# Optimization experiments

Measured on AMD Instinct MI355X. Metric: run time of the kernel, lower is better.

## Reference

```python
import jax, jax.numpy as jnp
import numpy as np
import math

D_MODEL = 256
NUM_SLOTS = 128
RANK = 32
STEPS = 6
VOCAB = 32000
SEQ = 512
BATCH = 8
LN_EPS = 1e-5


def setup_inputs() -> dict:
    key = jax.random.key(0)
    ks = jax.random.split(key, 16)
    std = 0.02
    inp = {
        "input_ids": jax.random.randint(ks[0], (BATCH, SEQ), 0, VOCAB),
        "attention_mask": jnp.ones((BATCH, SEQ), dtype=jnp.int32),
        "token_emb": jax.random.normal(ks[1], (VOCAB, D_MODEL), jnp.float32) * std,
        "pos_emb": jax.random.normal(ks[2], (SEQ, D_MODEL), jnp.float32) * std,
        "H": jax.random.normal(ks[3], (NUM_SLOTS, D_MODEL), jnp.float32) / math.sqrt(D_MODEL),
        "W_source": jax.random.normal(ks[4], (NUM_SLOTS, NUM_SLOTS, D_MODEL, RANK), jnp.float32) * std,
        "W_target": jax.random.normal(ks[5], (NUM_SLOTS, NUM_SLOTS, RANK, D_MODEL), jnp.float32) * std,
        "Wq_in": jax.random.normal(ks[6], (D_MODEL, D_MODEL), jnp.float32) / math.sqrt(D_MODEL),
        "Wk_slots": jax.random.normal(ks[7], (D_MODEL, D_MODEL), jnp.float32) / math.sqrt(D_MODEL),
        "Wv_in": jax.random.normal(ks[8], (D_MODEL, D_MODEL), jnp.float32) / math.sqrt(D_MODEL),
        "Wq_out": jax.random.normal(ks[9], (D_MODEL, D_MODEL), jnp.float32) / math.sqrt(D_MODEL),
        "Wk_fin": jax.random.normal(ks[10], (D_MODEL, D_MODEL), jnp.float32) / math.sqrt(D_MODEL),
        "Wv_fin": jax.random.normal(ks[11], (D_MODEL, D_MODEL), jnp.float32) / math.sqrt(D_MODEL),
        "W_out_proj": jax.random.normal(ks[12], (VOCAB, D_MODEL), jnp.float32) / math.sqrt(D_MODEL),
        "ln_scale": jnp.ones((STEPS, D_MODEL), jnp.float32),
        "ln_bias": jnp.zeros((STEPS, D_MODEL), jnp.float32),
    }
    return inp


def _layernorm(x, g, b):
    mu = jnp.mean(x, axis=-1, keepdims=True)
    var = jnp.var(x, axis=-1, keepdims=True)
    return (x - mu) / jnp.sqrt(var + LN_EPS) * g + b


def _forward(input_ids, attention_mask, token_emb, pos_emb, H, W_source, W_target,
             Wq_in, Wk_slots, Wv_in, Wq_out, Wk_fin, Wv_fin, W_out_proj, ln_scale, ln_bias):
    B, L = input_ids.shape
    scale = 1.0 / math.sqrt(D_MODEL)
    # embeddings (dropout is identity in eval)
    X = token_emb[input_ids] + pos_emb[jnp.arange(L)][None]  # (B,L,D)
    # compress: input tokens -> slots
    Q_in = X @ Wq_in.T                      # (B,L,D)
    K_sl = H @ Wk_slots.T                   # (S,D)
    V_in = X @ Wv_in.T                      # (B,L,D)
    A = jax.nn.softmax(Q_in @ K_sl.T * scale, axis=-1)  # (B,L,S)
    m = attention_mask.astype(A.dtype)[..., None]
    A = A * m
    A = A / (jnp.sum(A, axis=1, keepdims=True) + 1e-8)
    IR = jnp.einsum('bls,bld->bsd', A, V_in)            # (B,S,D)
    H_state = H[None] + IR                               # (B,S,D)

    off_diag = (1.0 - jnp.eye(NUM_SLOTS, dtype=H_state.dtype))  # (S,S)

    def step(h, lnp):
        g, b = lnp
        # bilinear slot-to-slot influence; contract directly, no (B,S,S,D) expand of h
        inter = jnp.einsum('bid,ijdr->bijr', h, W_source)        # (B,S,S,R)
        out = jnp.einsum('bijr,ijrd->bijd', inter, W_target)     # (B,S,S,D)
        infl = jnp.einsum('bijd,ij->bjd', out, off_diag)         # mask diag + sum over i
        h = _layernorm(h + jax.nn.relu(infl), g, b)
        return h, None

    H_state, _ = jax.lax.scan(step, H_state, (ln_scale, ln_bias))

    # expand: slots -> tokens
    Q_out = X @ Wq_out.T                   # (B,L,D)
    K_f = H_state @ Wk_fin.T               # (B,S,D)
    V_f = H_state @ Wv_fin.T               # (B,S,D)
    A2 = jax.nn.softmax(jnp.einsum('bld,bsd->bls', Q_out, K_f) * scale, axis=-1)
    Y = jnp.einsum('bls,bsd->bld', A2, V_f)
    logits = Y @ W_out_proj.T              # (B,L,V)
    return logits


def reference(input_ids, attention_mask, token_emb, pos_emb, H, W_source, W_target,
              Wq_in, Wk_slots, Wv_in, Wq_out, Wk_fin, Wv_fin, W_out_proj, ln_scale, ln_bias):
    return _forward(input_ids, attention_mask, token_emb, pos_emb, H, W_source, W_target,
                    Wq_in, Wk_slots, Wv_in, Wq_out, Wk_fin, Wv_fin, W_out_proj, ln_scale, ln_bias)
```

## Files before the change

### kernel.cpp

```cpp
#include <hip/hip_runtime.h>
#include <hip/hip_bf16.h>
#include <math.h>

#define D_MODEL 256
#define NUM_SLOTS 128
#define RANK 32
#define N_STEPS 6
#define VOCAB 32000
#define SEQ 512
#define BATCH 8
#define NTOK (BATCH*SEQ)
#define LN_EPS 1e-5f
#define SM_SCALE 0.0625f
#define IGROUPS 8

#define CB_A 0
#define NC_A 15360
#define CB_B (CB_A + NC_A)
#define NC_B 11776
#define CB_C (CB_B + NC_B)
#define NC_C 19200
#define CB_D (CB_C + NC_C)
#define NC_D 19200

typedef __attribute__((ext_vector_type(8))) short bf16x8;
typedef __attribute__((ext_vector_type(8))) _Float16 f16x8;
typedef __attribute__((ext_vector_type(4))) float f32x4;

#define GLD_LDS16(g, l) __builtin_amdgcn_global_load_lds( \
    (const __attribute__((address_space(1))) unsigned int*)(g), \
    (__attribute__((address_space(3))) unsigned int*)(l), 16, 0, 0)

__device__ inline unsigned pk2(float a, float b) {
    auto v = __builtin_amdgcn_cvt_pkrtz(a, b);
    union { decltype(v) x; unsigned u; } c;
    c.x = v;
    return c.u;
}
__device__ inline unsigned short f2h(float x) {
    union { _Float16 h; unsigned short u; } c;
    c.h = (_Float16)x;
    return c.u;
}

__device__ __forceinline__ void dev_convert(int cb, int t, float* ldsAll,
        const float* __restrict__ Ws, const float* __restrict__ Wt,
        unsigned short* __restrict__ WF) {
    int z = cb >> 14, i = (cb >> 7) & 127, j = cb & 127;
    int w = t >> 6, l = t & 63;
    float* lw = &ldsAll[w*1056];
    size_t sBase = ((size_t)i*128 + j)*8192;
    size_t pOut = ((size_t)j*128 + i)*16384;
    int g = l >> 4, c = l & 15;
    if (z < 2) {
        int ks = z*4 + w;
        const float4* s4 = (const float4*)(Ws + sBase) + ks*256;
        #pragma unroll
        for (int q = 0; q < 4; ++q) {
            int idx = q*64 + l;
            float4 v = s4[idx];
            *(float4*)&lw[(idx>>3)*33 + 4*(idx&7)] = v;
        }
        asm volatile("s_waitcnt lgkmcnt(0)" ::: "memory");
        bool diag = (i == j);
        #pragma unroll
        for (int mt = 0; mt < 2; ++mt) {
            union { f16x8 v; } o;
            #pragma unroll
            for (int e = 0; e < 8; ++e) {
                float f = diag ? 0.f : lw[(g*8 + e)*33 + mt*16 + c];
                o.v[e] = (_Float16)f;
            }
            *(f16x8*)(WF + pOut + (size_t)((ks*2 + mt)*64 + l)*8) = o.v;
        }
    } else {
        int p0 = (z - 2)*8 + w*2;
        const float4* s4 = (const float4*)(Wt + sBase);
        #pragma unroll
        for (int q = 0; q < 4; ++q) {
            int idx = q*64 + l;
            int r = idx >> 3, c8 = idx & 7;
            float4 v = s4[r*64 + p0*4 + c8];
            *(float4*)&lw[r*33 + 4*c8] = v;
        }
        asm volatile("s_waitcnt lgkmcnt(0)" ::: "memory");
        #pragma unroll
        for (int dn = 0; dn < 2; ++dn) {
            int nt = p0 + dn;
            union { f16x8 v; } o;
            #pragma unroll
            for (int e = 0; e < 8; ++e)
                o.v[e] = (_Float16)lw[(g*8 + e)*33 + dn*16 + c];
            *(f16x8*)(WF + pOut + 8192 + (size_t)(nt*64 + l)*8) = o.v;
        }
    }
}

__global__ __launch_bounds__(256) void k_front_a(const int* __restrict__ ids,
        const float* __restrict__ tok, const float* __restrict__ pos,
        const float* __restrict__ B0, const float* __restrict__ B1,
        const float* __restrict__ B2, float* __restrict__ C0,
        float* __restrict__ C1, float* __restrict__ C2,
        const float* __restrict__ Ws, const float* __restrict__ Wt,
        unsigned short* __restrict__ WF) {
    __shared__ float smem[4352];
    int bid = blockIdx.x;
    int t = threadIdx.x;
    if (bid >= 768) { dev_convert(CB_A + bid - 768, t, smem, Ws, Wt, WF); return; }
    const int K = D_MODEL, N = D_MODEL;
    int bx = bid & 63, byz = bid >> 6;
    int by = byz & 3, bz = byz >> 2;
    const float* B = bz == 0 ? B0 : (bz == 1 ? B1 : B2);
    float* C = bz == 0 ? C0 : (bz == 1 ? C1 : C2);
    float* As = smem;
    float* Bs = smem + 2048;
    int* sid = (int*)(smem + 4096);
    int bm = bx * 64, bn = by * 64;
    if (t < 64) sid[t] = ids[bm + t];
    __syncthreads();
    int tm = (t & 15) * 4, tn = (t >> 4) * 4;
    float acc[4][4] = {};
    for (int k0 = 0; k0 < K; k0 += 32) {
        #pragma unroll
        for (int r = 0; r < 8; ++r) {
            int idx = r*256 + t;
            int m = idx >> 5, k = idx & 31;
            int gm = bm + m;
            As[k*64 + m] = tok[(size_t)sid[m]*K + k0 + k] + pos[(gm & (SEQ-1))*K + k0 + k];
        }
        #pragma unroll
        for (int r = 0; r < 8; ++r) {
            int idx = r*256 + t;
            int n = idx >> 5, k = idx & 31;
            Bs[k*64 + n] = B[(size_t)(bn+n)*K + k0 + k];
        }
        __syncthreads();
        #pragma unroll
        for (int k = 0; k < 32; ++k) {
            float4 a4 = *(const float4*)&As[k*64 + tm];
            float4 b4 = *(const float4*)&Bs[k*64 + tn];
            float a[4] = {a4.x,a4.y,a4.z,a4.w};
            float b[4] = {b4.x,b4.y,b4.z,b4.w};
            #pragma unroll
            for (int i = 0; i < 4; ++i)
                #pragma unroll
                for (int jj = 0; jj < 4; ++jj)
                    acc[i][jj] += a[i]*b[jj];
        }
        __syncthreads();
    }
    #pragma unroll
    for (int i = 0; i < 4; ++i) {
        float4 v = make_float4(acc[i][0],acc[i][1],acc[i][2],acc[i][3]);
        *(float4*)&C[(size_t)(bm+tm+i)*N + bn+tn] = v;
    }
}

__global__ __launch_bounds__(256) void k_front_b(const float* __restrict__ Hin,
        const float* __restrict__ Wk_sl, float* __restrict__ Ksl,
        const float* __restrict__ Wop, unsigned short* __restrict__ Wf16,
        const float* __restrict__ Ws, const float* __restrict__ Wt,
        unsigned short* __restrict__ WF) {
    __shared__ float smem[4352];
    int bid = blockIdx.x;
    int t = threadIdx.x;
    if (bid >= 8008) { dev_convert(CB_B + bid - 8008, t, smem, Ws, Wt, WF); return; }
    if (bid >= 8) {
        int i = (bid - 8)*256 + t;
        float4 v = ((const float4*)Wop)[i];
        ushort4 h;
        h.x = f2h(v.x); h.y = f2h(v.y); h.z = f2h(v.z); h.w = f2h(v.w);
        ((ushort4*)Wf16)[i] = h;
        return;
    }
    const int K = D_MODEL, N = D_MODEL;
    int bx = bid & 1, by = bid >> 1;
    float* As = smem;
    float* Bs = smem + 2048;
    int bm = bx * 64, bn = by * 64;
    int tm = (t & 15) * 4, tn = (t >> 4) * 4;
    float acc[4][4] = {};
    for (int k0 = 0; k0 < K; k0 += 32) {
        #pragma unroll
        for (int r = 0; r < 8; ++r) {
            int idx = r*256 + t;
            int m = idx >> 5, k = idx & 31;
            As[k*64 + m] = Hin[(size_t)(bm+m)*K + k0 + k];
        }
        #pragma unroll
        for (int r = 0; r < 8; ++r) {
            int idx = r*256 + t;
            int n = idx >> 5, k = idx & 31;
            Bs[k*64 + n] = Wk_sl[(size_t)(bn+n)*K + k0 + k];
        }
        __syncthreads();
        #pragma unroll
        for (int k = 0; k < 32; ++k) {
            float4 a4 = *(const float4*)&As[k*64 + tm];
            float4 b4 = *(const float4*)&Bs[k*64 + tn];
            float a[4] = {a4.x,a4.y,a4.z,a4.w};
            float b[4] = {b4.x,b4.y,b4.z,b4.w};
            #pragma unroll
            for (int i = 0; i < 4; ++i)
                #pragma unroll
                for (int jj = 0; jj < 4; ++jj)
                    acc[i][jj] += a[i]*b[jj];
        }
        __syncthreads();
    }
    #pragma unroll
    for (int i = 0; i < 4; ++i) {
        float4 v = make_float4(acc[i][0],acc[i][1],acc[i][2],acc[i][3]);
        *(float4*)&Ksl[(size_t)(bm+tm+i)*N + bn+tn] = v;
    }
}

__global__ __launch_bounds__(256) void k_front_c(const float* __restrict__ Qin,
        const float* __restrict__ Ksl, const int* __restrict__ mask,
        float* __restrict__ A,
        const float* __restrict__ Ws, const float* __restrict__ Wt,
        unsigned short* __restrict__ WF) {
    __shared__ float smem[4352];
    int bid = blockIdx.x;
    int t = threadIdx.x;
    if (bid >= NTOK) { dev_convert(CB_C + bid - NTOK, t, smem, Ws, Wt, WF); return; }
    int bl = bid;
    float* q   = smem;
    float* prt = smem + 256;
    float* red = smem + 512;
    q[t] = Qin[(size_t)bl*D_MODEL + t];
    __syncthreads();
    int s = t & 127, hf = t >> 7;
    const float* kr = Ksl + (size_t)s*D_MODEL + hf*128;
    float accp = 0.f;
    #pragma unroll 8
    for (int d = 0; d < 128; ++d) accp += q[hf*128 + d]*kr[d];
    prt[hf*128 + s] = accp;
    __syncthreads();
    float v = 0.f;
    if (t < 128) { v = (prt[t] + prt[128 + t]) * SM_SCALE; red[t] = v; }
    __syncthreads();
    for (int o = 64; o > 0; o >>= 1) { if (t < o) red[t] = fmaxf(red[t], red[t+o]); __syncthreads(); }
    float mx = red[0]; __syncthreads();
    float e = 0.f;
    if (t < 128) { e = expf(v - mx); red[t] = e; }
    __syncthreads();
    for (int o = 64; o > 0; o >>= 1) { if (t < o) red[t] += red[t+o]; __syncthreads(); }
    float sum = red[0];
    if (t < 128) {
        float m = (float)mask[bl];
        A[(size_t)bl*NUM_SLOTS + t] = e / sum * m;
    }
}

__global__ __launch_bounds__(256) void k_front_d(const float* __restrict__ A,
        const float* __restrict__ V, const float* __restrict__ H,
        float* __restrict__ Hs, unsigned short* __restrict__ Hs16,
        const float* __restrict__ Ws, const float* __restrict__ Wt,
        unsigned short* __restrict__ WF) {
    __shared__ float smem[4352];
    int bid = blockIdx.x;
    int t = threadIdx.x;
    if (bid >= BATCH*NUM_SLOTS) { dev_convert(CB_D + bid - BATCH*NUM_SLOTS, t, smem, Ws, Wt, WF); return; }
    int bs = bid; int b = bs >> 7; int s = bs & 127;
    int d = t;
    const float* Ab = A + (size_t)b*SEQ*NUM_SLOTS + s;
    const float* Vb = V + (size_t)b*SEQ*D_MODEL + d;
    float a0 = 0.f, a1 = 0.f, a2 = 0.f, a3 = 0.f;
    float s0 = 0.f, s1 = 0.f, s2 = 0.f, s3 = 0.f;
    for (int l = 0; l < SEQ; l += 4) {
        float w0 = Ab[(size_t)(l+0)*NUM_SLOTS];
        float w1 = Ab[(size_t)(l+1)*NUM_SLOTS];
        float w2 = Ab[(size_t)(l+2)*NUM_SLOTS];
        float w3 = Ab[(size_t)(l+3)*NUM_SLOTS];
        a0 += w0 * Vb[(size_t)(l+0)*D_MODEL];
        a1 += w1 * Vb[(size_t)(l+1)*D_MODEL];
        a2 += w2 * Vb[(size_t)(l+2)*D_MODEL];
        a3 += w3 * Vb[(size_t)(l+3)*D_MODEL];
        s0 += w0; s1 += w1; s2 += w2; s3 += w3;
    }
    float asum = (s0+s1) + (s2+s3) + 1e-8f;
    float acc = (a0+a1) + (a2+a3);
    float v = H[s*D_MODEL + d] + acc / asum;
    Hs[(size_t)bs*D_MODEL + d] = v;
    Hs16[(size_t)bs*D_MODEL + d] = f2h(v);
}

__global__ __launch_bounds__(256) void k_logits(
        const unsigned short* __restrict__ Ahg,
        const unsigned short* __restrict__ Bhg, float* __restrict__ C) {
    __shared__ unsigned short lds[2*8192];
    int bm = blockIdx.x * 128, bn = blockIdx.y * 128;
    int t = threadIdx.x;
    int w = t >> 6, l = t & 63;
    int wr = w >> 1, wc = w & 1;
    int lr = l & 15, lk = l >> 4;
    f32x4 acc[4][4];
    #pragma unroll
    for (int mi = 0; mi < 4; ++mi)
        #pragma unroll
        for (int ni = 0; ni < 4; ++ni)
            acc[mi][ni] = (f32x4){0.f,0.f,0.f,0.f};

    for (int kc = 0; kc < 4; ++kc) {
        if (kc) __syncthreads();
        #pragma unroll
        for (int i = 0; i < 4; ++i) {
            int c = t + i*256;
            int row = c >> 3, c8 = c & 7;
            size_t ga = (size_t)(bm+row)*256 + kc*64 + c8*8;
            size_t gb = (size_t)(bn+row)*256 + kc*64 + c8*8;
            GLD_LDS16(Ahg + ga, &lds[c*8]);
            GLD_LDS16(Bhg + gb, &lds[8192 + c*8]);
        }
        __syncthreads();
        #pragma unroll
        for (int s = 0; s < 2; ++s) {
            f16x8 ah[4], bh[4];
            #pragma unroll
            for (int mi = 0; mi < 4; ++mi) {
                int off = (wr*64 + mi*16 + lr)*64 + s*32 + lk*8;
                ah[mi] = *(const f16x8*)&lds[off];
            }
            #pragma unroll
            for (int ni = 0; ni < 4; ++ni) {
                int off = (wc*64 + ni*16 + lr)*64 + s*32 + lk*8;
                bh[ni] = *(const f16x8*)&lds[8192 + off];
            }
            #pragma unroll
            for (int mi = 0; mi < 4; ++mi)
                #pragma unroll
                for (int ni = 0; ni < 4; ++ni)
                    acc[mi][ni] = __builtin_amdgcn_mfma_f32_16x16x32_f16(ah[mi], bh[ni], acc[mi][ni], 0, 0, 0);
        }
    }
    #pragma unroll
    for (int mi = 0; mi < 4; ++mi)
        #pragma unroll
        for (int ni = 0; ni < 4; ++ni) {
            int col = bn + wc*64 + ni*16 + lr;
            #pragma unroll
            for (int r = 0; r < 4; ++r) {
                int row = bm + wr*64 + mi*16 + lk*4 + r;
                C[(size_t)row*VOCAB + col] = acc[mi][ni][r];
            }
        }
}

__global__ __launch_bounds__(256, 4) void k_pairs_mfma(const unsigned short* __restrict__ h16,
        const unsigned short* __restrict__ WF, float* __restrict__ part) {
    __shared__ unsigned short lds[2*10240];
    int j = blockIdx.x, g = blockIdx.y;
    int t = threadIdx.x, w = t >> 6, l = t & 63;
    int lg = l >> 4, c = l & 15;
    const unsigned short* pbase = WF + ((size_t)j*128 + g*16)*16384;

    {
        const unsigned short* src = pbase;
        #pragma unroll
        for (int q = 0; q < 4; ++q)
            GLD_LDS16(src + (size_t)(q*256 + t)*8, &lds[(q*256 + t)*8]);
        const unsigned short* hsrc = h16 + ((size_t)(t&7)*NUM_SLOTS + g*16)*D_MODEL + (t>>3)*8;
        GLD_LDS16(hsrc, &lds[8192 + t*8]);
    }
    __builtin_amdgcn_sched_barrier(0);
    f16x8 bqn[4];
    #pragma unroll
    for (int nt = 0; nt < 4; ++nt)
        bqn[nt] = *(const f16x8*)(pbase + 8192 + (size_t)((w*4+nt)*64 + l)*8);
    __builtin_amdgcn_sched_barrier(0);

    f32x4 acc[4];
    #pragma unroll
    for (int nt = 0; nt < 4; ++nt) acc[nt] = (f32x4){0.f,0.f,0.f,0.f};
    f16x8 hzero;
    #pragma unroll
    for (int e = 0; e < 8; ++e) hzero[e] = (_Float16)0.f;

    #pragma unroll 2
    for (int ii = 0; ii < 16; ++ii) {
        int cur = ii & 1;
        asm volatile("s_waitcnt vmcnt(4) lgkmcnt(0)" ::: "memory");
        __builtin_amdgcn_s_barrier();
        __builtin_amdgcn_sched_barrier(0);
        if (ii < 15) {
            const unsigned short* src = pbase + (size_t)(ii+1)*16384;
            unsigned short* dst = &lds[(cur^1)*10240];
            #pragma unroll
            for (int q = 0; q < 4; ++q)
                GLD_LDS16(src + (size_t)(q*256 + t)*8, dst + (size_t)(q*256 + t)*8);
            const unsigned short* hsrc = h16 + ((size_t)(t&7)*NUM_SLOTS + (g*16+ii+1))*D_MODEL + (t>>3)*8;
            GLD_LDS16(hsrc, dst + 8192 + (size_t)t*8);
        }
        __builtin_amdgcn_sched_barrier(0);
        f16x8 bq[4];
        #pragma unroll
        for (int nt = 0; nt < 4; ++nt) bq[nt] = bqn[nt];
        if (ii < 15) {
            const unsigned short* bp = pbase + (size_t)(ii+1)*16384 + 8192;
            #pragma unroll
            for (int nt = 0; nt < 4; ++nt)
                bqn[nt] = *(const f16x8*)(bp + (size_t)((w*4+nt)*64 + l)*8);
        }
        const unsigned short* buf = &lds[cur*10240];
        f32x4 d1[2];
        d1[0] = (f32x4){0.f,0.f,0.f,0.f};
        d1[1] = (f32x4){0.f,0.f,0.f,0.f};
        #pragma unroll
        for (int ks = 0; ks < 8; ++ks) {
            f16x8 a0 = *(const f16x8*)(buf + (size_t)((ks*2+0)*64 + l)*8);
            f16x8 a1 = *(const f16x8*)(buf + (size_t)((ks*2+1)*64 + l)*8);
            f16x8 hv = *(const f16x8*)(buf + 8192 + (size_t)(((ks*4+lg)*8 + (c&7)))*8);
            f16x8 hb = (c < 8) ? hv : hzero;
            d1[0] = __builtin_amdgcn_mfma_f32_16x16x32_f16(a0, hb, d1[0], 0, 0, 0);
            d1[1] = __builtin_amdgcn_mfma_f32_16x16x32_f16(a1, hb, d1[1], 0, 0, 0);
        }
        unsigned q0 = pk2(d1[0][0], d1[0][1]);
        unsigned q1 = pk2(d1[0][2], d1[0][3]);
        unsigned s0 = pk2(d1[1][0], d1[1][1]);
        unsigned s1 = pk2(d1[1][2], d1[1][3]);
        int srcLo = 32*(lg & 1) + c;
        int srcHi = srcLo + 16;
        unsigned a0s = (unsigned)__shfl((int)q0, srcLo, 64);
        unsigned a1s = (unsigned)__shfl((int)q1, srcLo, 64);
        unsigned a2s = (unsigned)__shfl((int)q0, srcHi, 64);
        unsigned a3s = (unsigned)__shfl((int)q1, srcHi, 64);
        unsigned b0s = (unsigned)__shfl((int)s0, srcLo, 64);
        unsigned b1s = (unsigned)__shfl((int)s1, srcLo, 64);
        unsigned b2s = (unsigned)__shfl((int)s0, srcHi, 64);
        unsigned b3s = (unsigned)__shfl((int)s1, srcHi, 64);
        bool himt = ((lg >> 1) & 1);
        union { unsigned u[4]; f16x8 v; } A2u;
        A2u.u[0] = himt ? b0s : a0s;
        A2u.u[1] = himt ? b1s : a1s;
        A2u.u[2] = himt ? b2s : a2s;
        A2u.u[3] = himt ? b3s : a3s;
        #pragma unroll
        for (int nt = 0; nt < 4; ++nt)
            acc[nt] = __builtin_amdgcn_mfma_f32_16x16x32_f16(A2u.v, bq[nt], acc[nt], 0, 0, 0);
    }
    if (lg < 2) {
        #pragma unroll
        for (int nt = 0; nt < 4; ++nt) {
            int d = (w*4 + nt)*16 + c;
            #pragma unroll
            for (int r = 0; r < 4; ++r) {
                int b = lg*4 + r;
                part[(((size_t)g*BATCH + b)*NUM_SLOTS + j)*D_MODEL + d] = acc[nt][r];
            }
        }
    }
}

__global__ __launch_bounds__(256) void k_ln(float* __restrict__ h,
        unsigned short* __restrict__ h16, const float* __restrict__ part,
        const float* __restrict__ gma, const float* __restrict__ bta) {
    int bj = blockIdx.x;
    int t = threadIdx.x;
    int b = bj >> 7, j = bj & 127;
    __shared__ float red[256];
    float v = 0.f;
    #pragma unroll
    for (int g = 0; g < IGROUPS; ++g)
        v += part[(((size_t)g*BATCH + b)*NUM_SLOTS + j)*D_MODEL + t];
    float x = h[(size_t)bj*D_MODEL + t] + fmaxf(v, 0.f);
    red[t] = x; __syncthreads();
    for (int o = 128; o > 0; o >>= 1) { if (t < o) red[t] += red[t+o]; __syncthreads(); }
    float mu = red[0] * (1.0f/D_MODEL); __syncthreads();
    float dx = x - mu;
    red[t] = dx*dx; __syncthreads();
    for (int o = 128; o > 0; o >>= 1) { if (t < o) red[t] += red[t+o]; __syncthreads(); }
    float var = red[0] * (1.0f/D_MODEL);
    float outv = dx * rsqrtf(var + LN_EPS) * gma[t] + bta[t];
    h[(size_t)bj*D_MODEL + t] = outv;
    h16[(size_t)bj*D_MODEL + t] = f2h(outv);
}

__global__ __launch_bounds__(256) void k_kfvf(const float* __restrict__ A,
        const float* __restrict__ B0, const float* __restrict__ B1,
        float* __restrict__ C0, float* __restrict__ C1) {
    const int K = D_MODEL, N = D_MODEL;
    const float* B = blockIdx.z == 0 ? B0 : B1;
    float* C = blockIdx.z == 0 ? C0 : C1;
    __shared__ float As[32][64];
    __shared__ float Bs[32][64];
    int bm = blockIdx.x * 64, bn = blockIdx.y * 64;
    int t = threadIdx.x;
    int tm = (t & 15) * 4, tn = (t >> 4) * 4;
    float acc[4][4] = {};
    for (int k0 = 0; k0 < K; k0 += 32) {
        #pragma unroll
        for (int r = 0; r < 8; ++r) {
            int idx = r*256 + t;
            int m = idx >> 5, k = idx & 31;
            As[k][m] = A[(size_t)(bm+m)*K + k0 + k];
        }
        #pragma unroll
        for (int r = 0; r < 8; ++r) {
            int idx = r*256 + t;
            int n = idx >> 5, k = idx & 31;
            Bs[k][n] = B[(size_t)(bn+n)*K + k0 + k];
        }
        __syncthreads();
        #pragma unroll
        for (int k = 0; k < 32; ++k) {
            float4 a4 = *(const float4*)&As[k][tm];
            float4 b4 = *(const float4*)&Bs[k][tn];
            float a[4] = {a4.x,a4.y,a4.z,a4.w};
            float b[4] = {b4.x,b4.y,b4.z,b4.w};
            #pragma unroll
            for (int i = 0; i < 4; ++i)
                #pragma unroll
                for (int jj = 0; jj < 4; ++jj)
                    acc[i][jj] += a[i]*b[jj];
        }
        __syncthreads();
    }
    #pragma unroll
    for (int i = 0; i < 4; ++i) {
        float4 v = make_float4(acc[i][0],acc[i][1],acc[i][2],acc[i][3]);
        *(float4*)&C[(size_t)(bm+tm+i)*N + bn+tn] = v;
    }
}

__global__ __launch_bounds__(256) void k_attn2y(const float* __restrict__ Q,
        const float* __restrict__ Kf, const float* __restrict__ Vf,
        unsigned short* __restrict__ Yh) {
    int bl = blockIdx.x; int b = bl / SEQ;
    int t = threadIdx.x;
    __shared__ float q[D_MODEL];
    __shared__ float prt[2][128];
    __shared__ float a[128];
    __shared__ float red[128];
    q[t] = Q[(size_t)bl*D_MODEL + t];
    __syncthreads();
    int s = t & 127, hf = t >> 7;
    const float* kf = Kf + ((size_t)b*NUM_SLOTS + s)*D_MODEL + hf*128;
    float accp = 0.f;
    #pragma unroll 8
    for (int d = 0; d < 128; ++d) accp += q[hf*128 + d]*kf[d];
    prt[hf][s] = accp;
    __syncthreads();
    float v = 0.f;
    if (t < 128) { v = (prt[0][t] + prt[1][t]) * SM_SCALE; red[t] = v; }
    __syncthreads();
    for (int o = 64; o > 0; o >>= 1) { if (t < o) red[t] = fmaxf(red[t], red[t+o]); __syncthreads(); }
    float mx = red[0]; __syncthreads();
    if (t < 128) { float e = expf(v - mx); a[t] = e; red[t] = e; }
    __syncthreads();
    for (int o = 64; o > 0; o >>= 1) { if (t < o) red[t] += red[t+o]; __syncthreads(); }
    float inv = 1.0f / red[0];
    __syncthreads();
    const float* vf = Vf + (size_t)b*NUM_SLOTS*D_MODEL + t;
    float y0 = 0.f, y1 = 0.f, y2 = 0.f, y3 = 0.f;
    #pragma unroll
    for (int s2 = 0; s2 < NUM_SLOTS; s2 += 4) {
        y0 += a[s2+0]*vf[(size_t)(s2+0)*D_MODEL];
        y1 += a[s2+1]*vf[(size_t)(s2+1)*D_MODEL];
        y2 += a[s2+2]*vf[(size_t)(s2+2)*D_MODEL];
        y3 += a[s2+3]*vf[(size_t)(s2+3)*D_MODEL];
    }
    float y = ((y0+y1) + (y2+y3)) * inv;
    Yh[(size_t)bl*D_MODEL + t] = f2h(y);
}

extern "C" void kernel_launch(void* const* d_in, const int* in_sizes, int n_in,
                              void* d_out, int out_size, void* d_ws, size_t ws_size,
                              hipStream_t stream) {
    const int*   ids    = (const int*)d_in[0];
    const int*   amask  = (const int*)d_in[1];
    const float* tok    = (const float*)d_in[2];
    const float* pos    = (const float*)d_in[3];
    const float* Hin    = (const float*)d_in[4];
    const float* Ws     = (const float*)d_in[5];
    const float* Wt     = (const float*)d_in[6];
    const float* Wq_in  = (const float*)d_in[7];
    const float* Wk_sl  = (const float*)d_in[8];
    const float* Wv_in  = (const float*)d_in[9];
    const float* Wq_out = (const float*)d_in[10];
    const float* Wk_fin = (const float*)d_in[11];
    const float* Wv_fin = (const float*)d_in[12];
    const float* Wop    = (const float*)d_in[13];
    const float* lnsc   = (const float*)d_in[14];
    const float* lnbs   = (const float*)d_in[15];
    float* out = (float*)d_out;

    const size_t WF_USH = (size_t)16384 * 16384;
    unsigned short* WF = (unsigned short*)d_ws;
    float* ws = (float*)(WF + WF_USH);

    float* X    = ws;
    float* Qin  = X    + (size_t)NTOK*D_MODEL;
    float* Vin  = Qin  + (size_t)NTOK*D_MODEL;
    float* Ksl  = Vin  + (size_t)NTOK*D_MODEL;
    float* Asc  = Ksl  + (size_t)NUM_SLOTS*D_MODEL;
    float* csp  = Asc  + (size_t)NTOK*NUM_SLOTS;
    float* Hst  = csp  + (size_t)BATCH*8*NUM_SLOTS;
    float* part = Hst  + (size_t)BATCH*NUM_SLOTS*D_MODEL;
    float* Qout = part + (size_t)IGROUPS*BATCH*NUM_SLOTS*D_MODEL;
    float* Kf   = Qout + (size_t)NTOK*D_MODEL;
    float* Vf   = Kf   + (size_t)BATCH*NUM_SLOTS*D_MODEL;
    float* A2   = Vf   + (size_t)BATCH*NUM_SLOTS*D_MODEL;
    float* Yb   = A2   + (size_t)NTOK*NUM_SLOTS;
    unsigned short* Yh = (unsigned short*)(Yb + (size_t)NTOK*D_MODEL);
    unsigned short* Yl = Yh + (size_t)NTOK*D_MODEL;
    unsigned short* Wf16 = Yl + (size_t)NTOK*D_MODEL;
    unsigned short* Hst16 = Wf16 + (size_t)VOCAB*D_MODEL;

    k_front_a<<<768 + NC_A, 256, 0, stream>>>(ids, tok, pos,
            Wq_in, Wv_in, Wq_out, Qin, Vin, Qout, Ws, Wt, WF);
    k_front_b<<<8008 + NC_B, 256, 0, stream>>>(Hin, Wk_sl, Ksl, Wop, Wf16, Ws, Wt, WF);
    k_front_c<<<NTOK + NC_C, 256, 0, stream>>>(Qin, Ksl, amask, Asc, Ws, Wt, WF);
    k_front_d<<<BATCH*NUM_SLOTS + NC_D, 256, 0, stream>>>(Asc, Vin, Hin, Hst, Hst16, Ws, Wt, WF);

    for (int st = 0; st < N_STEPS; ++st) {
        k_pairs_mfma<<<dim3(NUM_SLOTS, IGROUPS), 256, 0, stream>>>(Hst16, WF, part);
        k_ln<<<BATCH*NUM_SLOTS, 256, 0, stream>>>(Hst, Hst16, part, lnsc + st*D_MODEL, lnbs + st*D_MODEL);
    }
    k_kfvf<<<dim3(BATCH*NUM_SLOTS/64, 4, 2), 256, 0, stream>>>(Hst, Wk_fin, Wv_fin, Kf, Vf);
    k_attn2y<<<NTOK, 256, 0, stream>>>(Qout, Kf, Vf, Yh);
    k_logits<<<dim3(NTOK/128, VOCAB/128), 256, 0, stream>>>(Yh, Wf16, out);
}
```

Measured before the change: 1.352 ms.

## Fuse layernorm into pairs kernel via last-block ticket reduction

Removes the separate k_ln launch per step. Each (j, group) block of the pairs kernel writes its partial, then bumps a per-slot atomic ticket, and the last of the IGROUPS blocks reduces all partials and runs the layernorm for that slot across every batch. The fp16 copy of the slot state is double-buffered so later blocks in the same step still read the old state. This saves six kernel launches and their gaps, at the cost of atomics, fences and a serial tail of layernorm work done by one block per slot.

Result: slower. 2.546 ms (+88.4%).

```diff
diff --git a/kernel.cpp b/kernel.cpp
--- a/kernel.cpp
+++ b/kernel.cpp
@@ -102,11 +102,12 @@
         const float* __restrict__ B2, float* __restrict__ C0,
         float* __restrict__ C1, float* __restrict__ C2,
         const float* __restrict__ Ws, const float* __restrict__ Wt,
-        unsigned short* __restrict__ WF) {
+        unsigned short* __restrict__ WF, unsigned* __restrict__ ticket) {
     __shared__ float smem[4352];
     int bid = blockIdx.x;
     int t = threadIdx.x;
     if (bid >= 768) { dev_convert(CB_A + bid - 768, t, smem, Ws, Wt, WF); return; }
+    if (bid == 0 && t < NUM_SLOTS) ticket[t] = 0u;
     const int K = D_MODEL, N = D_MODEL;
     int bx = bid & 63, byz = bid >> 6;
     int by = byz & 3, bz = byz >> 2;
@@ -347,8 +348,11 @@
         }
 }
 
-__global__ __launch_bounds__(256, 4) void k_pairs_mfma(const unsigned short* __restrict__ h16,
-        const unsigned short* __restrict__ WF, float* __restrict__ part) {
+__global__ __launch_bounds__(256, 4) void k_pairs_mfma(const unsigned short* __restrict__ h16in,
+        const unsigned short* __restrict__ WF, float* __restrict__ part,
+        float* __restrict__ Hst, unsigned short* __restrict__ h16out,
+        const float* __restrict__ gma, const float* __restrict__ bta,
+        unsigned* __restrict__ ticket) {
     __shared__ unsigned short lds[2*10240];
     int j = blockIdx.x, g = blockIdx.y;
     int t = threadIdx.x, w = t >> 6, l = t & 63;
@@ -360,7 +364,7 @@
         #pragma unroll
         for (int q = 0; q < 4; ++q)
             GLD_LDS16(src + (size_t)(q*256 + t)*8, &lds[(q*256 + t)*8]);
-        const unsigned short* hsrc = h16 + ((size_t)(t&7)*NUM_SLOTS + g*16)*D_MODEL + (t>>3)*8;
+        const unsigned short* hsrc = h16in + ((size_t)(t&7)*NUM_SLOTS + g*16)*D_MODEL + (t>>3)*8;
         GLD_LDS16(hsrc, &lds[8192 + t*8]);
     }
     __builtin_amdgcn_sched_barrier(0);
@@ -389,7 +393,7 @@
             #pragma unroll
             for (int q = 0; q < 4; ++q)
                 GLD_LDS16(src + (size_t)(q*256 + t)*8, dst + (size_t)(q*256 + t)*8);
-            const unsigned short* hsrc = h16 + ((size_t)(t&7)*NUM_SLOTS + (g*16+ii+1))*D_MODEL + (t>>3)*8;
+            const unsigned short* hsrc = h16in + ((size_t)(t&7)*NUM_SLOTS + (g*16+ii+1))*D_MODEL + (t>>3)*8;
             GLD_LDS16(hsrc, dst + 8192 + (size_t)t*8);
         }
         __builtin_amdgcn_sched_barrier(0);
@@ -450,30 +454,38 @@
             }
         }
     }
-}
-
-__global__ __launch_bounds__(256) void k_ln(float* __restrict__ h,
-        unsigned short* __restrict__ h16, const float* __restrict__ part,
-        const float* __restrict__ gma, const float* __restrict__ bta) {
-    int bj = blockIdx.x;
-    int t = threadIdx.x;
-    int b = bj >> 7, j = bj & 127;
-    __shared__ float red[256];
-    float v = 0.f;
-    #pragma unroll
-    for (int g = 0; g < IGROUPS; ++g)
-        v += part[(((size_t)g*BATCH + b)*NUM_SLOTS + j)*D_MODEL + t];
-    float x = h[(size_t)bj*D_MODEL + t] + fmaxf(v, 0.f);
-    red[t] = x; __syncthreads();
-    for (int o = 128; o > 0; o >>= 1) { if (t < o) red[t] += red[t+o]; __syncthreads(); }
-    float mu = red[0] * (1.0f/D_MODEL); __syncthreads();
-    float dx = x - mu;
-    red[t] = dx*dx; __syncthreads();
-    for (int o = 128; o > 0; o >>= 1) { if (t < o) red[t] += red[t+o]; __syncthreads(); }
-    float var = red[0] * (1.0f/D_MODEL);
-    float outv = dx * rsqrtf(var + LN_EPS) * gma[t] + bta[t];
-    h[(size_t)bj*D_MODEL + t] = outv;
-    h16[(size_t)bj*D_MODEL + t] = f2h(outv);
+    __threadfence();
+    __syncthreads();
+    __shared__ unsigned lastFlag;
+    if (t == 0) {
+        unsigned prev = atomicAdd(&ticket[j], 1u);
+        lastFlag = (prev == IGROUPS - 1) ? 1u : 0u;
+    }
+    __syncthreads();
+    if (lastFlag) {
+        if (t == 0) atomicExch(&ticket[j], 0u);
+        __threadfence();
+        float* red = (float*)lds;
+        for (int b = 0; b < BATCH; ++b) {
+            int bj = b*NUM_SLOTS + j;
+            float v = 0.f;
+            #pragma unroll
+            for (int g2 = 0; g2 < IGROUPS; ++g2)
+                v += part[(((size_t)g2*BATCH + b)*NUM_SLOTS + j)*D_MODEL + t];
+            float x = Hst[(size_t)bj*D_MODEL + t] + fmaxf(v, 0.f);
+            red[t] = x; __syncthreads();
+            for (int o = 128; o > 0; o >>= 1) { if (t < o) red[t] += red[t+o]; __syncthreads(); }
+            float mu = red[0] * (1.0f/D_MODEL); __syncthreads();
+            float dx = x - mu;
+            red[t] = dx*dx; __syncthreads();
+            for (int o = 128; o > 0; o >>= 1) { if (t < o) red[t] += red[t+o]; __syncthreads(); }
+            float var = red[0] * (1.0f/D_MODEL);
+            float outv = dx * rsqrtf(var + LN_EPS) * gma[t] + bta[t];
+            Hst[(size_t)bj*D_MODEL + t] = outv;
+            h16out[(size_t)bj*D_MODEL + t] = f2h(outv);
+            __syncthreads();
+        }
+    }
 }
 
 __global__ __launch_bounds__(256) void k_kfvf(const float* __restrict__ A,
@@ -605,18 +617,23 @@
     unsigned short* Yh = (unsigned short*)(Yb + (size_t)NTOK*D_MODEL);
     unsigned short* Yl = Yh + (size_t)NTOK*D_MODEL;
     unsigned short* Wf16 = Yl + (size_t)NTOK*D_MODEL;
-    unsigned short* Hst16 = Wf16 + (size_t)VOCAB*D_MODEL;
+    unsigned short* Hst16A = Wf16 + (size_t)VOCAB*D_MODEL;
+    unsigned short* Hst16B = Hst16A + (size_t)BATCH*NUM_SLOTS*D_MODEL;
+    unsigned* ticket = (unsigned*)(Hst16B + (size_t)BATCH*NUM_SLOTS*D_MODEL);
 
     k_front_a<<<768 + NC_A, 256, 0, stream>>>(ids, tok, pos,
-            Wq_in, Wv_in, Wq_out, Qin, Vin, Qout, Ws, Wt, WF);
+            Wq_in, Wv_in, Wq_out, Qin, Vin, Qout, Ws, Wt, WF, ticket);
     k_front_b<<<8008 + NC_B, 256, 0, stream>>>(Hin, Wk_sl, Ksl, Wop, Wf16, Ws, Wt, WF);
     k_front_c<<<NTOK + NC_C, 256, 0, stream>>>(Qin, Ksl, amask, Asc, Ws, Wt, WF);
-    k_front_d<<<BATCH*NUM_SLOTS + NC_D, 256, 0, stream>>>(Asc, Vin, Hin, Hst, Hst16, Ws, Wt, WF);
+    k_front_d<<<BATCH*NUM_SLOTS + NC_D, 256, 0, stream>>>(Asc, Vin, Hin, Hst, Hst16A, Ws, Wt, WF);
 
     for (int st = 0; st < N_STEPS; ++st) {
-        k_pairs_mfma<<<dim3(NUM_SLOTS, IGROUPS), 256, 0, stream>>>(Hst16, WF, part);
-        k_ln<<<BATCH*NUM_SLOTS, 256, 0, stream>>>(Hst, Hst16, part, lnsc + st*D_MODEL, lnbs + st*D_MODEL);
-    }
+        unsigned short* hin  = (st & 1) ? Hst16B : Hst16A;
+        unsigned short* hout = (st & 1) ? Hst16A : Hst16B;
+        k_pairs_mfma<<<dim3(NUM_SLOTS, IGROUPS), 256, 0, stream>>>(hin, WF, part,
+                Hst, hout, lnsc + st*D_MODEL, lnbs + st*D_MODEL, ticket);
+    }
+
     k_kfvf<<<dim3(BATCH*NUM_SLOTS/64, 4, 2), 256, 0, stream>>>(Hst, Wk_fin, Wv_fin, Kf, Vf);
     k_attn2y<<<NTOK, 256, 0, stream>>>(Qout, Kf, Vf, Yh);
     k_logits<<<dim3(NTOK/128, VOCAB/128), 256, 0, stream>>>(Yh, Wf16, out);
```
